# Optimization experiments

Hardware: AMD Instinct MI355X
Metric: run time of the kernel (lower is better)

Reference implementation:

```python
import jax, jax.numpy as jnp
import numpy as np


def setup_inputs() -> dict:
    key = jax.random.key(0)
    k1, k2 = jax.random.split(key)
    x = jax.random.normal(k1, (4, 1, 16384), dtype=jnp.float32)  # [B, C, T]
    # dictionary initialized uniform(-1, 1) as in nn.Parameter(...).uniform_(-1, 1)
    d = jax.random.uniform(k2, (256, 1, 256), dtype=jnp.float32, minval=-1.0, maxval=1.0)  # [A, C, K]
    return {"x": x, "d": d, "n_iterations": 16}


def reference(x, d, n_iterations):
    B, C, T = x.shape
    A, _, K = d.shape
    pad = K // 2
    # normalize each atom over (channels, atom_size) dims, i.e. d_normalization_dims=(-1,-2)
    norms = jnp.linalg.norm(d.reshape(A, -1), axis=-1)
    dn = d / (norms[:, None, None] + 1e-12)

    # work in a padded domain so conv output position == start index in padded residual
    rp = jnp.pad(x, ((0, 0), (0, 0), (pad, pad)))        # residual, [B, C, T+2*pad]
    recon = jnp.zeros_like(rp)                            # accumulated reconstruction
    Tout = T + 2 * pad - K + 1                            # conv output length

    def step(carry, _):
        rp, recon = carry
        # cross-correlation of residual with every atom: [B, A, Tout]
        fm = jax.lax.conv_general_dilated(
            rp, dn, window_strides=(1,), padding='VALID',
            dimension_numbers=('NCH', 'OIH', 'NCH'))
        flat = fm.reshape(B, A * Tout)
        idx = jnp.argmax(flat, axis=-1)                   # signed max, per batch item
        val = jnp.take_along_axis(flat, idx[:, None], axis=-1)[:, 0]
        atom_idx = idx // Tout
        pos = idx % Tout                                  # start index in padded domain
        atoms = dn[atom_idx] * val[:, None, None]         # [B, C, K]

        def upd(r, rec, a, p):
            seg = jax.lax.dynamic_slice(r, (0, p), (C, K))
            r2 = jax.lax.dynamic_update_slice(r, seg - a, (0, p))
            segr = jax.lax.dynamic_slice(rec, (0, p), (C, K))
            rec2 = jax.lax.dynamic_update_slice(rec, segr + a, (0, p))
            return r2, rec2

        rp2, recon2 = jax.vmap(upd)(rp, recon, atoms, pos)
        return (rp2, recon2), None

    (rp, recon), _ = jax.lax.scan(step, (rp, recon), None, length=n_iterations)
    # crop padding -> reconstruction with same shape as x
    return recon[:, :, pad:pad + T]
```

## Files before the change

### kernel.cpp

```cpp
#include <hip/hip_runtime.h>
#include <math.h>

#define B    4
#define T    16384
#define A    256
#define K    256
#define PAD  128
#define TP   (T + 2*PAD)
#define TOUT (TP - K + 1)
#define ITERS 16
#define CHUNK 512
#define NCHUNK 33
#define NCP  36
#define TILE 2048
#define NTILE 9
#define NBLK 512
#define BPB  128
#define BARSTRIDE 64

struct Smem {
    float rp[TILE + K + 16];
    float dnA[K];
    float dnB[K];
    float dnsel[K];
    float wv[16]; int wi[16];
    float fv; int fi;
};

#define TAP(acc, s0,s1,s2,s3, dq) { acc = fmaf(s0,(dq).x,acc); acc = fmaf(s1,(dq).y,acc); \
                                    acc = fmaf(s2,(dq).z,acc); acc = fmaf(s3,(dq).w,acc); }

__device__ __forceinline__ void wave_amax(float& bv, int& bi) {
    #pragma unroll
    for (int off = 32; off; off >>= 1) {
        float ov = __shfl_down(bv, off);
        int   oi = __shfl_down(bi, off);
        if (ov > bv || (ov == bv && oi < bi)) { bv = ov; bi = oi; }
    }
}

__device__ __forceinline__ void gbar(unsigned* c, unsigned target) {
    __syncthreads();
    if (threadIdx.x == 0) {
        __hip_atomic_fetch_add(c, 1u, __ATOMIC_RELEASE, __HIP_MEMORY_SCOPE_AGENT);
        while (__hip_atomic_load(c, __ATOMIC_RELAXED, __HIP_MEMORY_SCOPE_AGENT) < target)
            __builtin_amdgcn_s_sleep(2);
        (void)__hip_atomic_load(c, __ATOMIC_ACQUIRE, __HIP_MEMORY_SCOPE_AGENT);
    }
    __syncthreads();
}

__device__ __forceinline__ void dev_norm(int a0, int tid, const float* __restrict__ d,
                                         float* __restrict__ dn, Smem& sm) {
    int lane = tid & 63, w = tid >> 6;
    #pragma unroll
    for (int s = 0; s < 2; s++) {
        int atom = a0*2 + s;
        float v = d[atom*K + tid];
        float sq = v*v;
        #pragma unroll
        for (int off = 32; off; off >>= 1) sq += __shfl_down(sq, off);
        if (lane == 0) sm.wv[w] = sq;
        __syncthreads();
        float norm = sqrtf(sm.wv[0] + sm.wv[1] + sm.wv[2] + sm.wv[3]) + 1e-12f;
        dn[atom*K + tid] = v / norm;
        __syncthreads();
    }
}

__device__ __forceinline__ void dev_init(int a0, int b, int tid, const float* __restrict__ x,
                                         float* __restrict__ rp, float* __restrict__ recon) {
    int i = a0*256 + tid;
    if (i < TP) {
        float v = (i >= PAD && i < PAD + T) ? x[b*T + (i - PAD)] : 0.f;
        rp[(size_t)b*TP + i] = v;
        recon[(size_t)b*TP + i] = 0.f;
    }
}

__device__ void dev_conv(int a0, int b, int tid, const float* __restrict__ rp,
                         const float* __restrict__ dn,
                         float* __restrict__ segval, int* __restrict__ segidx,
                         float* __restrict__ abv, int* __restrict__ abi, Smem& sm) {
    const int aA = a0*2, aB = a0*2 + 1;
    const int lane = tid & 63, w = tid >> 6;
    sm.dnA[tid] = dn[aA*K + tid];
    sm.dnB[tid] = dn[aB*K + tid];
    const float4* rp4 = (const float4*)(rp + (size_t)b*TP);

    for (int tile = 0; tile < NTILE; tile++) {
        int t0 = tile * TILE;
        __syncthreads();
        float4* s4 = (float4*)sm.rp;
        for (int i = tid; i < 580; i += 256) {
            int g = t0/4 + i;
            float4 v = {0.f,0.f,0.f,0.f};
            if (g*4 < TP) v = rp4[g];
            s4[i] = v;
        }
        __syncthreads();
        const float4* srp4 = (const float4*)sm.rp;
        const float4* dA4  = (const float4*)sm.dnA;
        const float4* dB4  = (const float4*)sm.dnB;
        float accA0[4] = {0,0,0,0}, accA1[4] = {0,0,0,0};
        float accB0[4] = {0,0,0,0}, accB1[4] = {0,0,0,0};
        float4 p = srp4[tid];
        float4 q = srp4[tid + 256];
        #pragma unroll 4
        for (int kq = 0; kq < 64; kq++) {
            float4 dA = dA4[kq];
            float4 dB = dB4[kq];
            float4 pn = srp4[tid + kq + 1];
            float4 qn = srp4[tid + 256 + kq + 1];
            TAP(accA0[0], p.x,p.y,p.z,p.w, dA); TAP(accA0[1], p.y,p.z,p.w,pn.x, dA);
            TAP(accA0[2], p.z,p.w,pn.x,pn.y, dA); TAP(accA0[3], p.w,pn.x,pn.y,pn.z, dA);
            TAP(accB0[0], p.x,p.y,p.z,p.w, dB); TAP(accB0[1], p.y,p.z,p.w,pn.x, dB);
            TAP(accB0[2], p.z,p.w,pn.x,pn.y, dB); TAP(accB0[3], p.w,pn.x,pn.y,pn.z, dB);
            TAP(accA1[0], q.x,q.y,q.z,q.w, dA); TAP(accA1[1], q.y,q.z,q.w,qn.x, dA);
            TAP(accA1[2], q.z,q.w,qn.x,qn.y, dA); TAP(accA1[3], q.w,qn.x,qn.y,qn.z, dA);
            TAP(accB1[0], q.x,q.y,q.z,q.w, dB); TAP(accB1[1], q.y,q.z,q.w,qn.x, dB);
            TAP(accB1[2], q.z,q.w,qn.x,qn.y, dB); TAP(accB1[3], q.w,qn.x,qn.y,qn.z, dB);
            p = pn; q = qn;
        }
        int lt = tid * 4;
        float bvA0 = -INFINITY, bvA1 = -INFINITY, bvB0 = -INFINITY, bvB1 = -INFINITY;
        int biA0 = 0x7fffffff, biA1 = 0x7fffffff, biB0 = 0x7fffffff, biB1 = 0x7fffffff;
        #pragma unroll
        for (int j = 0; j < 4; j++) {
            int t = t0 + lt + j;
            if (t < TOUT) {
                if (accA0[j] > bvA0) { bvA0 = accA0[j]; biA0 = aA*TOUT + t; }
                if (accB0[j] > bvB0) { bvB0 = accB0[j]; biB0 = aB*TOUT + t; }
            }
            int t1 = t0 + 1024 + lt + j;
            if (t1 < TOUT) {
                if (accA1[j] > bvA1) { bvA1 = accA1[j]; biA1 = aA*TOUT + t1; }
                if (accB1[j] > bvB1) { bvB1 = accB1[j]; biB1 = aB*TOUT + t1; }
            }
        }
        wave_amax(bvA0, biA0); wave_amax(bvA1, biA1);
        wave_amax(bvB0, biB0); wave_amax(bvB1, biB1);
        if (lane == 0) {
            sm.wv[w]    = bvA0; sm.wi[w]    = biA0;
            sm.wv[4+w]  = bvA1; sm.wi[4+w]  = biA1;
            sm.wv[8+w]  = bvB0; sm.wi[8+w]  = biB0;
            sm.wv[12+w] = bvB1; sm.wi[12+w] = biB1;
        }
        __syncthreads();
        if (tid < 4) {
            float v0 = sm.wv[2*tid];   int i0 = sm.wi[2*tid];
            float v1 = sm.wv[2*tid+1]; int i1 = sm.wi[2*tid+1];
            if (v1 > v0 || (v1 == v0 && i1 < i0)) { v0 = v1; i0 = i1; }
            int chunk = tile*4 + tid;
            if (chunk < NCHUNK) {
                segval[((size_t)b*A + aA)*NCP + chunk] = v0;
                segidx[((size_t)b*A + aA)*NCP + chunk] = i0;
            }
        } else if (tid >= 64 && tid < 68) {
            int c = tid - 64;
            float v0 = sm.wv[8+2*c];   int i0 = sm.wi[8+2*c];
            float v1 = sm.wv[8+2*c+1]; int i1 = sm.wi[8+2*c+1];
            if (v1 > v0 || (v1 == v0 && i1 < i0)) { v0 = v1; i0 = i1; }
            int chunk = tile*4 + c;
            if (chunk < NCHUNK) {
                segval[((size_t)b*A + aB)*NCP + chunk] = v0;
                segidx[((size_t)b*A + aB)*NCP + chunk] = i0;
            }
        }
    }
    __syncthreads();
    if (w < 2) {
        int atom = (w == 0) ? aA : aB;
        float bv = -INFINITY; int bi = 0x7fffffff;
        if (lane < NCHUNK) {
            bv = segval[((size_t)b*A + atom)*NCP + lane];
            bi = segidx[((size_t)b*A + atom)*NCP + lane];
        }
        wave_amax(bv, bi);
        if (lane == 0) { abv[b*A + atom] = bv; abi[b*A + atom] = bi; }
    }
}

__device__ void dev_iter(int a0, int b, int tid, int last,
                         const float* __restrict__ avc, const int* __restrict__ aic,
                         float* __restrict__ avn, int* __restrict__ ain,
                         const float* __restrict__ rin, float* __restrict__ rout,
                         float* __restrict__ recon, const float* __restrict__ dn,
                         float* __restrict__ segval, int* __restrict__ segidx, Smem& sm) {
    const int aA = a0*2, aB = a0*2 + 1;
    const int lane = tid & 63, w = tid >> 6;

    float bv0 = avc[b*A + tid]; int bi0 = aic[b*A + tid];
    const float4* rin4 = (const float4*)(rin + (size_t)b*TP);
    const int icopy = a0*256 + tid;
    const bool docopy = (!last) && (icopy < TP/4);
    float4 vcopy = {0.f,0.f,0.f,0.f};
    if (docopy) vcopy = rin4[icopy];
    sm.dnA[tid] = dn[aA*K + tid];
    sm.dnB[tid] = dn[aB*K + tid];

    {
        float bv = bv0; int bi = bi0;
        wave_amax(bv, bi);
        if (lane == 0) { sm.wv[w] = bv; sm.wi[w] = bi; }
        __syncthreads();
        if (tid == 0) {
            bv = sm.wv[0]; bi = sm.wi[0];
            for (int j = 1; j < 4; j++)
                if (sm.wv[j] > bv || (sm.wv[j] == bv && sm.wi[j] < bi)) { bv = sm.wv[j]; bi = sm.wi[j]; }
            sm.fv = bv; sm.fi = bi;
        }
        __syncthreads();
    }
    float val = sm.fv; int idx = sm.fi;
    int atom = idx / TOUT, pos = idx - atom*TOUT;
    sm.dnsel[tid] = dn[atom*K + tid];

    int lo = pos - (K-1); if (lo < 0) lo = 0;
    int c_lo = lo >> 9;
    int tbase = c_lo * CHUNK;

    if (!last) {
        float4* s4 = (float4*)sm.rp;
        for (int i = tid; i < 324; i += 256) {
            int g = tbase/4 + i;
            float4 v = {0.f,0.f,0.f,0.f};
            if (g*4 < TP) v = rin4[g];
            s4[i] = v;
        }
    }
    __syncthreads();
    if (docopy) {
        float4* rout4 = (float4*)(rout + (size_t)b*TP);
        float4 v = vcopy;
        int o = icopy*4 - pos;
        if (o > -4 && o < K) {
            if (o+0 >= 0 && o+0 < K) v.x -= val * sm.dnsel[o+0];
            if (o+1 >= 0 && o+1 < K) v.y -= val * sm.dnsel[o+1];
            if (o+2 >= 0 && o+2 < K) v.z -= val * sm.dnsel[o+2];
            if (o+3 >= 0 && o+3 < K) v.w -= val * sm.dnsel[o+3];
        }
        rout4[icopy] = v;
    }
    if (a0 == 0) {
        recon[(size_t)b*TP + pos + tid] += val * sm.dnsel[tid];
    }
    if (last) return;

    sm.rp[pos + tid - tbase] -= val * sm.dnsel[tid];
    __syncthreads();

    const float4* srp4 = (const float4*)sm.rp;
    const float4* dA4  = (const float4*)sm.dnA;
    const float4* dB4  = (const float4*)sm.dnB;
    float cA[4] = {0,0,0,0}, cB[4] = {0,0,0,0};
    float4 p = srp4[tid];
    #pragma unroll 4
    for (int kq = 0; kq < 64; kq++) {
        float4 dA = dA4[kq];
        float4 dB = dB4[kq];
        float4 pn = srp4[tid + kq + 1];
        TAP(cA[0], p.x,p.y,p.z,p.w, dA); TAP(cA[1], p.y,p.z,p.w,pn.x, dA);
        TAP(cA[2], p.z,p.w,pn.x,pn.y, dA); TAP(cA[3], p.w,pn.x,pn.y,pn.z, dA);
        TAP(cB[0], p.x,p.y,p.z,p.w, dB); TAP(cB[1], p.y,p.z,p.w,pn.x, dB);
        TAP(cB[2], p.z,p.w,pn.x,pn.y, dB); TAP(cB[3], p.w,pn.x,pn.y,pn.z, dB);
        p = pn;
    }
    int lt = tid * 4;
    float bvA = -INFINITY, bvB = -INFINITY;
    int biA = 0x7fffffff, biB = 0x7fffffff;
    #pragma unroll
    for (int j = 0; j < 4; j++) {
        int t = tbase + lt + j;
        if (t < TOUT) {
            if (cA[j] > bvA) { bvA = cA[j]; biA = aA*TOUT + t; }
            if (cB[j] > bvB) { bvB = cB[j]; biB = aB*TOUT + t; }
        }
    }
    wave_amax(bvA, biA); wave_amax(bvB, biB);
    if (lane == 0) { sm.wv[w] = bvA; sm.wi[w] = biA; sm.wv[8+w] = bvB; sm.wi[8+w] = biB; }
    __syncthreads();
    if (tid < 2) {
        float v0 = sm.wv[2*tid];   int i0 = sm.wi[2*tid];
        float v1 = sm.wv[2*tid+1]; int i1 = sm.wi[2*tid+1];
        if (v1 > v0 || (v1 == v0 && i1 < i0)) { v0 = v1; i0 = i1; }
        int chunk = c_lo + tid;
        if (chunk < NCHUNK) {
            segval[((size_t)b*A + aA)*NCP + chunk] = v0;
            segidx[((size_t)b*A + aA)*NCP + chunk] = i0;
        }
    } else if (tid >= 64 && tid < 66) {
        int c = tid - 64;
        float v0 = sm.wv[8+2*c];   int i0 = sm.wi[8+2*c];
        float v1 = sm.wv[8+2*c+1]; int i1 = sm.wi[8+2*c+1];
        if (v1 > v0 || (v1 == v0 && i1 < i0)) { v0 = v1; i0 = i1; }
        int chunk = c_lo + c;
        if (chunk < NCHUNK) {
            segval[((size_t)b*A + aB)*NCP + chunk] = v0;
            segidx[((size_t)b*A + aB)*NCP + chunk] = i0;
        }
    }
    __syncthreads();
    if (w < 2) {
        int at = (w == 0) ? aA : aB;
        float bv = -INFINITY; int bi = 0x7fffffff;
        if (lane < NCHUNK) {
            bv = segval[((size_t)b*A + at)*NCP + lane];
            bi = segidx[((size_t)b*A + at)*NCP + lane];
        }
        wave_amax(bv, bi);
        if (lane == 0) { avn[b*A + at] = bv; ain[b*A + at] = bi; }
    }
}

__global__ void __launch_bounds__(256, 2)
k_coop(const float* __restrict__ x, const float* __restrict__ d, float* __restrict__ out,
       float* __restrict__ dn, float* __restrict__ rp0, float* __restrict__ rp1,
       float* __restrict__ recon, float* __restrict__ segval, int* __restrict__ segidx,
       float* __restrict__ abv0, int* __restrict__ abi0,
       float* __restrict__ abv1, int* __restrict__ abi1, unsigned* __restrict__ bar) {
    __shared__ Smem sm;
    const int bid = blockIdx.x, tid = threadIdx.x;
    const int a0 = bid & 127, b = bid >> 7;
    unsigned* cb = bar + b*BARSTRIDE;
    unsigned gen = 0;
    dev_norm(a0, tid, d, dn, sm);
    dev_init(a0, b, tid, x, rp0, recon);
    gen++; gbar(cb, gen*BPB);
    dev_conv(a0, b, tid, rp0, dn, segval, segidx, abv0, abi0, sm);
    gen++; gbar(cb, gen*BPB);
    const float* rin = rp0; float* rout = rp1;
    const float* avc = abv0; const int* aic = abi0;
    float* avn = abv1; int* ain = abi1;
    for (int it = 0; it < ITERS-1; it++) {
        dev_iter(a0, b, tid, 0, avc, aic, avn, ain,
                 rin, rout, recon, dn, segval, segidx, sm);
        { const float* t1 = rin; rin = rout; rout = (float*)t1; }
        { const float* t2 = avc; avc = avn; avn = (float*)t2; }
        { const int*   t3 = aic; aic = ain; ain = (int*)t3; }
        gen++; gbar(cb, gen*BPB);
    }
    if (a0 == 0) {
        dev_iter(a0, b, tid, 1, avc, aic, avn, ain,
                 rin, rout, recon, dn, segval, segidx, sm);
        const float4* rc4 = (const float4*)(recon + (size_t)b*TP + PAD);
        float4* o4 = (float4*)(out + (size_t)b*T);
        for (int i = tid; i < T/4; i += 256) o4[i] = rc4[i];
    }
}

__global__ void __launch_bounds__(256) k_f_norm_init(const float* x, const float* d,
                                                     float* dn, float* rp0, float* recon) {
    __shared__ Smem sm;
    dev_norm(blockIdx.x & 127, threadIdx.x, d, dn, sm);
    dev_init(blockIdx.x & 127, blockIdx.x >> 7, threadIdx.x, x, rp0, recon);
}
__global__ void __launch_bounds__(256, 2) k_f_conv(const float* rp, const float* dn,
                                                   float* segval, int* segidx,
                                                   float* abv, int* abi) {
    __shared__ Smem sm;
    dev_conv(blockIdx.x & 127, blockIdx.x >> 7, threadIdx.x, rp, dn, segval, segidx, abv, abi, sm);
}
__global__ void __launch_bounds__(256, 2) k_f_iter(int last,
                                                   const float* avc, const int* aic,
                                                   float* avn, int* ain,
                                                   const float* rin, float* rout,
                                                   float* recon, const float* dn,
                                                   float* segval, int* segidx) {
    __shared__ Smem sm;
    dev_iter(blockIdx.x & 127, blockIdx.x >> 7, threadIdx.x, last,
             avc, aic, avn, ain, rin, rout, recon, dn, segval, segidx, sm);
}
__global__ void k_f_out(const float* recon, float* out) {
    int i = blockIdx.x * blockDim.x + threadIdx.x;
    if (i >= B*T) return;
    int b = i / T, t = i - b*T;
    out[i] = recon[(size_t)b*TP + PAD + t];
}

extern "C" void kernel_launch(void* const* d_in, const int* in_sizes, int n_in,
                              void* d_out, int out_size, void* d_ws, size_t ws_size,
                              hipStream_t stream) {
    const float* x = (const float*)d_in[0];
    const float* d = (const float*)d_in[1];
    float* out = (float*)d_out;

    float* ws     = (float*)d_ws;
    float* dn     = ws;
    float* rp0    = dn  + (size_t)A*K;
    float* rp1    = rp0 + (size_t)B*TP;
    float* recon  = rp1 + (size_t)B*TP;
    float* segval = recon + (size_t)B*TP;
    int*   segidx = (int*)(segval + (size_t)B*A*NCP);
    float* abv0   = (float*)(segidx + (size_t)B*A*NCP);
    float* abv1   = abv0 + (size_t)B*A;
    int*   abi0   = (int*)(abv1 + (size_t)B*A);
    int*   abi1   = abi0 + (size_t)B*A;
    unsigned* bar = (unsigned*)(abi1 + (size_t)B*A);

    int nb = 0, ncu = 0;
    hipError_t e1 = hipOccupancyMaxActiveBlocksPerMultiprocessor(&nb, (const void*)k_coop, 256, 0);
    hipError_t e2 = hipDeviceGetAttribute(&ncu, hipDeviceAttributeMultiprocessorCount, 0);
    bool coop = (e1 == hipSuccess && e2 == hipSuccess && nb > 0 && ncu > 0 &&
                 (long)nb * ncu >= NBLK);
    if (coop) {
        (void)hipMemsetAsync(bar, 0, B*BARSTRIDE*sizeof(unsigned), stream);
        hipLaunchKernelGGL(k_coop, dim3(NBLK), dim3(256), 0, stream,
                           x, d, out, dn, rp0, rp1, recon,
                           segval, segidx, abv0, abi0, abv1, abi1, bar);
        return;
    }
    k_f_norm_init<<<NBLK, 256, 0, stream>>>(x, d, dn, rp0, recon);
    k_f_conv<<<NBLK, 256, 0, stream>>>(rp0, dn, segval, segidx, abv0, abi0);
    float* rbuf[2] = {rp0, rp1};
    float* av[2]   = {abv0, abv1};
    int*   ai[2]   = {abi0, abi1};
    for (int it = 0; it < ITERS; it++) {
        k_f_iter<<<NBLK, 256, 0, stream>>>(it == ITERS-1 ? 1 : 0,
                                           av[it & 1], ai[it & 1],
                                           av[(it + 1) & 1], ai[(it + 1) & 1],
                                           rbuf[it & 1], rbuf[(it + 1) & 1],
                                           recon, dn, segval, segidx);
    }
    k_f_out<<<(B*T + 255)/256, 256, 0, stream>>>(recon, out);
}
```

Measured before the change: 542.4 us.

## Keep full padded residual in LDS per block and recompute only affected chunks

Rewrites the persistent cooperative kernel so that each of 256 blocks holds the whole padded residual of its batch item in about 80KB of dynamic LDS and handles 4 atoms. Each block applies the selected atom update locally in LDS, then recomputes the correlation only for the 1024-sample window touching the update. This removes the global residual ping-pong, the recon buffer and the global segment max arrays, and halves the number of blocks taking part in each barrier. In exchange, occupancy drops to one block per CU, every block repeats the residual update redundantly, and the output is formed as x minus the final residual.

```diff
diff --git a/kernel.cpp b/kernel.cpp
--- a/kernel.cpp
+++ b/kernel.cpp
@@ -15,8 +15,199 @@
 #define TILE 2048
 #define NTILE 9
 #define NBLK 512
-#define BPB  128
+#define RPPAD 17664
+#define NBLK2 256
+#define BPB2 64
 #define BARSTRIDE 64
+#define DLDS 81920
+
+#define TAP(acc, s0,s1,s2,s3, dq) { acc = fmaf(s0,(dq).x,acc); acc = fmaf(s1,(dq).y,acc); \
+                                    acc = fmaf(s2,(dq).z,acc); acc = fmaf(s3,(dq).w,acc); }
+
+__device__ __forceinline__ void wave_amax(float& bv, int& bi) {
+    #pragma unroll
+    for (int off = 32; off; off >>= 1) {
+        float ov = __shfl_down(bv, off);
+        int   oi = __shfl_down(bi, off);
+        if (ov > bv || (ov == bv && oi < bi)) { bv = ov; bi = oi; }
+    }
+}
+
+struct KSmem {
+    float  rp[RPPAD];
+    float4 dn4[4][64];
+    float  chv[4][NCHUNK];
+    int    chi[4][NCHUNK];
+    float  wv[16]; int wi[16];
+    float  fv; int fi;
+};
+
+__device__ __forceinline__ void gbar64(unsigned* c, unsigned target, int tid) {
+    __syncthreads();
+    if (tid == 0) {
+        __hip_atomic_fetch_add(c, 1u, __ATOMIC_RELEASE, __HIP_MEMORY_SCOPE_AGENT);
+        while (__hip_atomic_load(c, __ATOMIC_RELAXED, __HIP_MEMORY_SCOPE_AGENT) < target)
+            __builtin_amdgcn_s_sleep(2);
+    }
+    __syncthreads();
+    __builtin_amdgcn_fence(__ATOMIC_ACQUIRE, "agent");
+}
+
+__device__ void region_update(KSmem& sm, int t0, int aBase, int tid) {
+    const int lane = tid & 63, w = tid >> 6;
+    const float4* srp4 = (const float4*)sm.rp;
+    float c0[4] = {0,0,0,0}, c1[4] = {0,0,0,0}, c2[4] = {0,0,0,0}, c3[4] = {0,0,0,0};
+    int base = (t0 >> 2) + tid;
+    float4 p = srp4[base];
+    #pragma unroll 4
+    for (int kq = 0; kq < 64; kq++) {
+        float4 d0 = sm.dn4[0][kq];
+        float4 d1 = sm.dn4[1][kq];
+        float4 d2 = sm.dn4[2][kq];
+        float4 d3 = sm.dn4[3][kq];
+        float4 pn = srp4[base + kq + 1];
+        TAP(c0[0], p.x,p.y,p.z,p.w, d0); TAP(c0[1], p.y,p.z,p.w,pn.x, d0);
+        TAP(c0[2], p.z,p.w,pn.x,pn.y, d0); TAP(c0[3], p.w,pn.x,pn.y,pn.z, d0);
+        TAP(c1[0], p.x,p.y,p.z,p.w, d1); TAP(c1[1], p.y,p.z,p.w,pn.x, d1);
+        TAP(c1[2], p.z,p.w,pn.x,pn.y, d1); TAP(c1[3], p.w,pn.x,pn.y,pn.z, d1);
+        TAP(c2[0], p.x,p.y,p.z,p.w, d2); TAP(c2[1], p.y,p.z,p.w,pn.x, d2);
+        TAP(c2[2], p.z,p.w,pn.x,pn.y, d2); TAP(c2[3], p.w,pn.x,pn.y,pn.z, d2);
+        TAP(c3[0], p.x,p.y,p.z,p.w, d3); TAP(c3[1], p.y,p.z,p.w,pn.x, d3);
+        TAP(c3[2], p.z,p.w,pn.x,pn.y, d3); TAP(c3[3], p.w,pn.x,pn.y,pn.z, d3);
+        p = pn;
+    }
+    int lt = t0 + tid*4;
+    float bv0 = -INFINITY, bv1 = -INFINITY, bv2 = -INFINITY, bv3 = -INFINITY;
+    int bi0 = 0x7fffffff, bi1 = 0x7fffffff, bi2 = 0x7fffffff, bi3 = 0x7fffffff;
+    #pragma unroll
+    for (int j = 0; j < 4; j++) {
+        int t = lt + j;
+        if (t < TOUT) {
+            if (c0[j] > bv0) { bv0 = c0[j]; bi0 = (aBase+0)*TOUT + t; }
+            if (c1[j] > bv1) { bv1 = c1[j]; bi1 = (aBase+1)*TOUT + t; }
+            if (c2[j] > bv2) { bv2 = c2[j]; bi2 = (aBase+2)*TOUT + t; }
+            if (c3[j] > bv3) { bv3 = c3[j]; bi3 = (aBase+3)*TOUT + t; }
+        }
+    }
+    wave_amax(bv0, bi0); wave_amax(bv1, bi1); wave_amax(bv2, bi2); wave_amax(bv3, bi3);
+    if (lane == 0) {
+        sm.wv[0*4+w] = bv0; sm.wi[0*4+w] = bi0;
+        sm.wv[1*4+w] = bv1; sm.wi[1*4+w] = bi1;
+        sm.wv[2*4+w] = bv2; sm.wi[2*4+w] = bi2;
+        sm.wv[3*4+w] = bv3; sm.wi[3*4+w] = bi3;
+    }
+    __syncthreads();
+    if (tid < 8) {
+        int a = tid >> 1, h = tid & 1;
+        float v0 = sm.wv[a*4 + 2*h];   int i0 = sm.wi[a*4 + 2*h];
+        float v1 = sm.wv[a*4 + 2*h+1]; int i1 = sm.wi[a*4 + 2*h+1];
+        if (v1 > v0 || (v1 == v0 && i1 < i0)) { v0 = v1; i0 = i1; }
+        int chunk = (t0 >> 9) + h;
+        if (chunk < NCHUNK) { sm.chv[a][chunk] = v0; sm.chi[a][chunk] = i0; }
+    }
+    __syncthreads();
+}
+
+__device__ __forceinline__ void best_write(KSmem& sm, int a0, int b, int tid,
+                                           float* __restrict__ abv, int* __restrict__ abi) {
+    const int lane = tid & 63, w = tid >> 6;
+    float bv = -INFINITY; int bi = 0x7fffffff;
+    if (lane < NCHUNK) { bv = sm.chv[w][lane]; bi = sm.chi[w][lane]; }
+    wave_amax(bv, bi);
+    if (lane == 0) { abv[b*A + a0*4 + w] = bv; abi[b*A + a0*4 + w] = bi; }
+}
+
+__device__ __forceinline__ void pick(KSmem& sm, int b, int tid,
+                                     const float* __restrict__ avc, const int* __restrict__ aic) {
+    const int lane = tid & 63, w = tid >> 6;
+    float bv = avc[b*A + tid]; int bi = aic[b*A + tid];
+    wave_amax(bv, bi);
+    if (lane == 0) { sm.wv[w] = bv; sm.wi[w] = bi; }
+    __syncthreads();
+    if (tid == 0) {
+        bv = sm.wv[0]; bi = sm.wi[0];
+        for (int j = 1; j < 4; j++)
+            if (sm.wv[j] > bv || (sm.wv[j] == bv && sm.wi[j] < bi)) { bv = sm.wv[j]; bi = sm.wi[j]; }
+        sm.fv = bv; sm.fi = bi;
+    }
+    __syncthreads();
+}
+
+__global__ void __launch_bounds__(256, 1)
+k_coop(const float* __restrict__ x, const float* __restrict__ d, float* __restrict__ out,
+       float* __restrict__ dn,
+       float* __restrict__ abv0, int* __restrict__ abi0,
+       float* __restrict__ abv1, int* __restrict__ abi1, unsigned* __restrict__ bar) {
+    extern __shared__ char raw[];
+    KSmem& sm = *(KSmem*)raw;
+    const int bid = blockIdx.x, tid = threadIdx.x;
+    const int a0 = bid & (BPB2-1), b = bid >> 6;
+    const int lane = tid & 63, w = tid >> 6;
+    unsigned* cb = bar + b*BARSTRIDE;
+
+    {
+        const float4* xb4 = (const float4*)(x + (size_t)b*T);
+        float4* rp4w = (float4*)sm.rp;
+        for (int i = tid; i < RPPAD/4; i += 256) {
+            float4 v = {0.f,0.f,0.f,0.f};
+            if (i >= PAD/4 && i < (PAD+T)/4) v = xb4[i - PAD/4];
+            rp4w[i] = v;
+        }
+    }
+    #pragma unroll
+    for (int s = 0; s < 4; s++) {
+        int atom = a0*4 + s;
+        float v = d[atom*K + tid];
+        float sq = v*v;
+        #pragma unroll
+        for (int off = 32; off; off >>= 1) sq += __shfl_down(sq, off);
+        if (lane == 0) sm.wv[w] = sq;
+        __syncthreads();
+        float norm = sqrtf(sm.wv[0] + sm.wv[1] + sm.wv[2] + sm.wv[3]) + 1e-12f;
+        float nv = v / norm;
+        ((float*)&sm.dn4[s][0])[tid] = nv;
+        dn[atom*K + tid] = nv;
+        __syncthreads();
+    }
+    for (int p = 0; p < 17; p++) region_update(sm, p*1024, a0*4, tid);
+    best_write(sm, a0, b, tid, abv0, abi0);
+    unsigned gen = 1; gbar64(cb, gen*BPB2, tid);
+
+    const float* avc = abv0; const int* aic = abi0;
+    float* avn = abv1; int* ain = abi1;
+    for (int it = 0; it < ITERS-1; it++) {
+        pick(sm, b, tid, avc, aic);
+        float val = sm.fv; int idx = sm.fi;
+        int atom = idx / TOUT, pos = idx - atom*TOUT;
+        float ds = dn[atom*K + tid];
+        sm.rp[pos + tid] -= val * ds;
+        __syncthreads();
+        int lo = pos - (K-1); if (lo < 0) lo = 0;
+        int t0 = (lo >> 9) * 512;
+        region_update(sm, t0, a0*4, tid);
+        best_write(sm, a0, b, tid, avn, ain);
+        { const float* t1 = avc; avc = avn; avn = (float*)t1; }
+        { const int*   t2 = aic; aic = ain; ain = (int*)t2; }
+        gen++; gbar64(cb, gen*BPB2, tid);
+    }
+    if (a0 == 0) {
+        pick(sm, b, tid, avc, aic);
+        float val = sm.fv; int idx = sm.fi;
+        int atom = idx / TOUT, pos = idx - atom*TOUT;
+        float ds = dn[atom*K + tid];
+        sm.rp[pos + tid] -= val * ds;
+        __syncthreads();
+        const float4* xb4 = (const float4*)(x + (size_t)b*T);
+        float4* o4 = (float4*)(out + (size_t)b*T);
+        for (int i = tid; i < T/4; i += 256) {
+            float4 xv = xb4[i];
+            float4 rv = *(const float4*)&sm.rp[PAD + i*4];
+            float4 ov; ov.x = xv.x - rv.x; ov.y = xv.y - rv.y;
+            ov.z = xv.z - rv.z; ov.w = xv.w - rv.w;
+            o4[i] = ov;
+        }
+    }
+}
 
 struct Smem {
     float rp[TILE + K + 16];
@@ -26,29 +217,6 @@
     float wv[16]; int wi[16];
     float fv; int fi;
 };
-
-#define TAP(acc, s0,s1,s2,s3, dq) { acc = fmaf(s0,(dq).x,acc); acc = fmaf(s1,(dq).y,acc); \
-                                    acc = fmaf(s2,(dq).z,acc); acc = fmaf(s3,(dq).w,acc); }
-
-__device__ __forceinline__ void wave_amax(float& bv, int& bi) {
-    #pragma unroll
-    for (int off = 32; off; off >>= 1) {
-        float ov = __shfl_down(bv, off);
-        int   oi = __shfl_down(bi, off);
-        if (ov > bv || (ov == bv && oi < bi)) { bv = ov; bi = oi; }
-    }
-}
-
-__device__ __forceinline__ void gbar(unsigned* c, unsigned target) {
-    __syncthreads();
-    if (threadIdx.x == 0) {
-        __hip_atomic_fetch_add(c, 1u, __ATOMIC_RELEASE, __HIP_MEMORY_SCOPE_AGENT);
-        while (__hip_atomic_load(c, __ATOMIC_RELAXED, __HIP_MEMORY_SCOPE_AGENT) < target)
-            __builtin_amdgcn_s_sleep(2);
-        (void)__hip_atomic_load(c, __ATOMIC_ACQUIRE, __HIP_MEMORY_SCOPE_AGENT);
-    }
-    __syncthreads();
-}
 
 __device__ __forceinline__ void dev_norm(int a0, int tid, const float* __restrict__ d,
                                          float* __restrict__ dn, Smem& sm) {
@@ -313,42 +481,6 @@
     }
 }
 
-__global__ void __launch_bounds__(256, 2)
-k_coop(const float* __restrict__ x, const float* __restrict__ d, float* __restrict__ out,
-       float* __restrict__ dn, float* __restrict__ rp0, float* __restrict__ rp1,
-       float* __restrict__ recon, float* __restrict__ segval, int* __restrict__ segidx,
-       float* __restrict__ abv0, int* __restrict__ abi0,
-       float* __restrict__ abv1, int* __restrict__ abi1, unsigned* __restrict__ bar) {
-    __shared__ Smem sm;
-    const int bid = blockIdx.x, tid = threadIdx.x;
-    const int a0 = bid & 127, b = bid >> 7;
-    unsigned* cb = bar + b*BARSTRIDE;
-    unsigned gen = 0;
-    dev_norm(a0, tid, d, dn, sm);
-    dev_init(a0, b, tid, x, rp0, recon);
-    gen++; gbar(cb, gen*BPB);
-    dev_conv(a0, b, tid, rp0, dn, segval, segidx, abv0, abi0, sm);
-    gen++; gbar(cb, gen*BPB);
-    const float* rin = rp0; float* rout = rp1;
-    const float* avc = abv0; const int* aic = abi0;
-    float* avn = abv1; int* ain = abi1;
-    for (int it = 0; it < ITERS-1; it++) {
-        dev_iter(a0, b, tid, 0, avc, aic, avn, ain,
-                 rin, rout, recon, dn, segval, segidx, sm);
-        { const float* t1 = rin; rin = rout; rout = (float*)t1; }
-        { const float* t2 = avc; avc = avn; avn = (float*)t2; }
-        { const int*   t3 = aic; aic = ain; ain = (int*)t3; }
-        gen++; gbar(cb, gen*BPB);
-    }
-    if (a0 == 0) {
-        dev_iter(a0, b, tid, 1, avc, aic, avn, ain,
-                 rin, rout, recon, dn, segval, segidx, sm);
-        const float4* rc4 = (const float4*)(recon + (size_t)b*TP + PAD);
-        float4* o4 = (float4*)(out + (size_t)b*T);
-        for (int i = tid; i < T/4; i += 256) o4[i] = rc4[i];
-    }
-}
-
 __global__ void __launch_bounds__(256) k_f_norm_init(const float* x, const float* d,
                                                      float* dn, float* rp0, float* recon) {
     __shared__ Smem sm;
@@ -398,16 +530,18 @@
     int*   abi1   = abi0 + (size_t)B*A;
     unsigned* bar = (unsigned*)(abi1 + (size_t)B*A);
 
+    (void)hipFuncSetAttribute((const void*)k_coop,
+                              hipFuncAttributeMaxDynamicSharedMemorySize, DLDS);
     int nb = 0, ncu = 0;
-    hipError_t e1 = hipOccupancyMaxActiveBlocksPerMultiprocessor(&nb, (const void*)k_coop, 256, 0);
+    hipError_t e1 = hipOccupancyMaxActiveBlocksPerMultiprocessor(&nb, (const void*)k_coop,
+                                                                 256, DLDS);
     hipError_t e2 = hipDeviceGetAttribute(&ncu, hipDeviceAttributeMultiprocessorCount, 0);
     bool coop = (e1 == hipSuccess && e2 == hipSuccess && nb > 0 && ncu > 0 &&
-                 (long)nb * ncu >= NBLK);
+                 (long)nb * ncu >= NBLK2);
     if (coop) {
         (void)hipMemsetAsync(bar, 0, B*BARSTRIDE*sizeof(unsigned), stream);
-        hipLaunchKernelGGL(k_coop, dim3(NBLK), dim3(256), 0, stream,
-                           x, d, out, dn, rp0, rp1, recon,
-                           segval, segidx, abv0, abi0, abv1, abi1, bar);
+        hipLaunchKernelGGL(k_coop, dim3(NBLK2), dim3(256), DLDS, stream,
+                           x, d, out, dn, abv0, abi0, abv1, abi1, bar);
         return;
     }
     k_f_norm_init<<<NBLK, 256, 0, stream>>>(x, d, dn, rp0, recon);
```

Result: slower. 700.9 us (+29.2%).
